# Performance work log

Measured on AMD Instinct MI355X. Metric: run time of the kernel, lower is better.

The kernel has to match this reference:

```python
import jax, jax.numpy as jnp
import numpy as np

NUM_HEADS = 16
DIM_HEAD = 64
DIM = 1024
SCALE = DIM ** (-0.5)  # NOTE: source scales by model dim, not dim_head


def setup_inputs() -> dict:
    key = jax.random.key(0)
    ks = jax.random.split(key, 6)
    b, n, d = 2, 2048, DIM
    return {
        "x": jax.random.normal(ks[0], (b, n, d), dtype=jnp.float32),
        "mask": jnp.ones((b, n), dtype=bool),
        "Wq": jax.random.normal(ks[1], (NUM_HEADS * DIM_HEAD, d), dtype=jnp.float32) * 0.02,
        "Wk": jax.random.normal(ks[2], (DIM_HEAD, d), dtype=jnp.float32) * 0.02,
        "Wv": jax.random.normal(ks[3], (DIM_HEAD, d), dtype=jnp.float32) * 0.02,
        "Wfc": jax.random.normal(ks[4], (d, NUM_HEADS * DIM_HEAD), dtype=jnp.float32) * 0.02,
        "bfc": jnp.zeros((d,), dtype=jnp.float32),
    }


def reference(x, mask, Wq, Wk, Wv, Wfc, bfc):
    b, n, _ = x.shape
    # projections (nn.Linear: y = x @ W.T)
    q = (x @ Wq.T).reshape(b, n, NUM_HEADS, DIM_HEAD).transpose(0, 2, 1, 3)  # b h n d
    k = x @ Wk.T  # b n d  (single shared MQA head)
    v = x @ Wv.T  # b n d
    energy = jnp.einsum("bhid,bjd->bhij", q, k) * SCALE  # b h i j
    mask_value = -jnp.finfo(energy.dtype).max
    # input mask: k_mask is all ones in source, so only query rows are masked
    q_mask = mask[:, None, :, None]  # b 1 i 1
    energy = jnp.where(q_mask, energy, mask_value)
    # causal mask: positions j > i are masked (i == j since self-attention)
    i = jnp.arange(n)
    causal = i[:, None] < i[None, :]  # True where future
    energy = jnp.where(causal[None, None, :, :], mask_value, energy)
    attn = jax.nn.softmax(energy, axis=-1)
    # dropout_rate = 0.0 -> identity
    out = jnp.einsum("bhij,bjd->bhid", attn, v)
    out = out.transpose(0, 2, 1, 3).reshape(b, n, NUM_HEADS * DIM_HEAD)
    return out @ Wfc.T + bfc
```

## Files before the change

### kernel.cpp

```cpp
#include <hip/hip_runtime.h>
#include <math.h>

#define NH 16
#define DH 64
#define DM 1024
#define NS 2048
#define BB 2
#define MR (BB * NS)
#define LDQ 1152
#define C_EXP 0.0450842201f

typedef unsigned short u16;
typedef __attribute__((ext_vector_type(8))) short short8;
typedef __attribute__((ext_vector_type(4))) float floatx4;
typedef __attribute__((ext_vector_type(4))) u16 u16x4;

#if __has_builtin(__builtin_amdgcn_exp2f)
#define EXP2(x) __builtin_amdgcn_exp2f(x)
#else
#define EXP2(x) exp2f(x)
#endif

#define MFMA16(a, b, c) __builtin_amdgcn_mfma_f32_16x16x32_bf16((a), (b), (c), 0, 0, 0)

static __device__ __forceinline__ u16 f2bf(float f) {
  union { float f; unsigned u; } v; v.f = f;
  unsigned r = v.u + 0x7fffu + ((v.u >> 16) & 1u);
  return (u16)(r >> 16);
}
static __device__ __forceinline__ u16 f2bf_fast(float f) {
  union { float f; unsigned u; } v; v.f = f;
  return (u16)((v.u + 0x8000u) >> 16);
}

#define GLDS16(gp, lp)                                                        \
  __builtin_amdgcn_global_load_lds(                                           \
      (const __attribute__((address_space(1))) void*)(const void*)(gp),       \
      (__attribute__((address_space(3))) void*)(void*)(lp), 16, 0, 0)

__global__ __launch_bounds__(256) void cast_all(
    const float* __restrict__ x, const float* __restrict__ wq,
    const float* __restrict__ wk, const float* __restrict__ wv,
    const float* __restrict__ wfc, u16* __restrict__ xb,
    u16* __restrict__ wqkvb, u16* __restrict__ wfcb) {
  const int NX = MR * DM / 4, NQ = DM * DM / 4, NK = DH * DM / 4;
  int id = blockIdx.x * 256 + threadIdx.x;
  const float* src;
  u16* dst;
  int off;
  if (id < NX) { src = x; dst = xb; off = id; }
  else if (id < NX + NQ) { src = wq; dst = wqkvb; off = id - NX; }
  else if (id < NX + NQ + NK) { src = wk; dst = wqkvb + (size_t)DM * DM; off = id - NX - NQ; }
  else if (id < NX + NQ + 2 * NK) { src = wv; dst = wqkvb + (size_t)(DM + DH) * DM; off = id - NX - NQ - NK; }
  else { src = wfc; dst = wfcb; off = id - NX - NQ - 2 * NK; }
  float4 f = ((const float4*)src)[off];
  u16x4 o;
  o[0] = f2bf(f.x); o[1] = f2bf(f.y); o[2] = f2bf(f.z); o[3] = f2bf(f.w);
  ((u16x4*)dst)[off] = o;
}

__global__ __launch_bounds__(256) void gemm64(
    const u16* __restrict__ A, const u16* __restrict__ W,
    const float* __restrict__ bias, void* __restrict__ Cout,
    u16* __restrict__ vT, int M, int N, int K, int ldc, int out_bf16,
    int v_by) {
  __shared__ u16 As[2][64 * 32];
  __shared__ u16 Ws[2][64 * 32];
  const int tid = threadIdx.x;
  const int lane = tid & 63;
  const int lr = lane & 15, quad = lane >> 4;
  const int wave = tid >> 6, wr = wave >> 1, wc = wave & 1;
  const int m0 = blockIdx.x * 64, n0 = blockIdx.y * 64;

  const int srow = tid >> 2;
  const int scg = (tid & 3) ^ ((srow >> 1) & 3);
  const u16* gA = A + (size_t)(m0 + srow) * K + scg * 8;
  const u16* gW = W + (size_t)(n0 + srow) * K + scg * 8;
  const int lo = wave * 512;

  floatx4 acc[2][2] = {};
  const int nt = K >> 5;

  GLDS16(gA, &As[0][lo]);
  GLDS16(gW, &Ws[0][lo]);

  for (int t = 0; t < nt; ++t) {
    __syncthreads();
    if (t + 1 < nt) {
      const int ko = (t + 1) << 5;
      const int nb = (t + 1) & 1;
      GLDS16(gA + ko, &As[nb][lo]);
      GLDS16(gW + ko, &Ws[nb][lo]);
    }
    const u16* as = As[t & 1];
    const u16* ws = Ws[t & 1];
    short8 af[2], wf[2];
#pragma unroll
    for (int mi = 0; mi < 2; ++mi) {
      int rr = wr * 32 + mi * 16 + lr;
      af[mi] = *(const short8*)&as[rr * 32 + ((quad ^ ((rr >> 1) & 3)) << 3)];
    }
#pragma unroll
    for (int nj = 0; nj < 2; ++nj) {
      int rc = wc * 32 + nj * 16 + lr;
      wf[nj] = *(const short8*)&ws[rc * 32 + ((quad ^ ((rc >> 1) & 3)) << 3)];
    }
#pragma unroll
    for (int mi = 0; mi < 2; ++mi)
#pragma unroll
      for (int nj = 0; nj < 2; ++nj)
        acc[mi][nj] = MFMA16(af[mi], wf[nj], acc[mi][nj]);
  }

  if (v_by >= 0 && (int)blockIdx.y == v_by) {
#pragma unroll
    for (int mi = 0; mi < 2; ++mi)
#pragma unroll
      for (int nj = 0; nj < 2; ++nj)
#pragma unroll
        for (int r = 0; r < 4; ++r)
          vT[(size_t)(wc * 32 + nj * 16 + lr) * MR + m0 + wr * 32 + mi * 16 +
             quad * 4 + r] = f2bf(acc[mi][nj][r]);
    return;
  }

#pragma unroll
  for (int mi = 0; mi < 2; ++mi) {
#pragma unroll
    for (int nj = 0; nj < 2; ++nj) {
      int col = n0 + wc * 32 + nj * 16 + lr;
      float badd = bias ? bias[col] : 0.f;
#pragma unroll
      for (int r = 0; r < 4; ++r) {
        int row = m0 + wr * 32 + mi * 16 + quad * 4 + r;
        float v = acc[mi][nj][r] + badd;
        if (out_bf16)
          ((u16*)Cout)[(size_t)row * ldc + col] = f2bf(v);
        else
          ((float*)Cout)[(size_t)row * ldc + col] = v;
      }
    }
  }
}

__global__ __launch_bounds__(128) void attn_mfma(
    const u16* __restrict__ qkv,
    const u16* __restrict__ vT,
    u16* __restrict__ aob) {
  __shared__ u16 Ks[2][64 * 64];
  __shared__ u16 Vt[2][64 * 64];
  __shared__ u16 Ps[2][16 * 72];

  const int b = blockIdx.z;
  const int p = blockIdx.x;
  const int head = blockIdx.y;
  const int tid = threadIdx.x;
  const int lane = tid & 63;
  const int lr = lane & 15, quad = lane >> 4;
  const int w = tid >> 6;
  const size_t rowb = (size_t)b * NS;
  const u16* kvK = qkv + rowb * LDQ + 1024;
  const u16* vTb = vT + rowb;

  int srow[4], scg[4];
#pragma unroll
  for (int g = 0; g < 4; ++g) {
    int ci = w * 256 + g * 64 + lane;
    srow[g] = ci >> 3;
    scg[g] = (ci & 7) ^ (srow[g] & 7);
  }

  for (int phase = 0; phase < 2; ++phase) {
    const int s = (phase == 0) ? (63 - p) : p;
    const int i0q = s * 32;
    const int ntp = (s >> 1) + 1;
    const int irow = i0q + w * 16 + quad * 4;

    const u16* qp = qkv + (rowb + i0q + w * 16 + lr) * LDQ + head * DH;
    short8 aq0 = *(const short8*)(qp + quad * 8);
    short8 aq1 = *(const short8*)(qp + 32 + quad * 8);

    floatx4 o[4] = {};
    float lacc[4] = {0.f, 0.f, 0.f, 0.f};

#pragma unroll
    for (int g = 0; g < 4; ++g)
      GLDS16(kvK + (size_t)srow[g] * LDQ + scg[g] * 8,
             &Ks[0][(w * 256 + g * 64) * 8]);
#pragma unroll
    for (int g = 0; g < 4; ++g)
      GLDS16(vTb + (size_t)srow[g] * MR + scg[g] * 8,
             &Vt[0][(w * 256 + g * 64) * 8]);

    for (int t = 0; t < ntp; ++t) {
      const int buf = t & 1;
      __syncthreads();

      if (t + 1 < ntp) {
        const int j0n = (t + 1) * 64;
        const int nb2 = buf ^ 1;
#pragma unroll
        for (int g = 0; g < 4; ++g)
          GLDS16(kvK + (size_t)(j0n + srow[g]) * LDQ + scg[g] * 8,
                 &Ks[nb2][(w * 256 + g * 64) * 8]);
#pragma unroll
        for (int g = 0; g < 4; ++g)
          GLDS16(vTb + (size_t)srow[g] * MR + j0n + scg[g] * 8,
                 &Vt[nb2][(w * 256 + g * 64) * 8]);
      }

      const int j0 = t * 64;
      const u16* ksb = Ks[buf];
      const u16* vtb = Vt[buf];
      floatx4 sv[4];
#pragma unroll
      for (int jb = 0; jb < 4; ++jb) {
        const int krow = jb * 16 + lr;
        short8 bk0 = *(const short8*)&ksb[krow * 64 + ((quad ^ (krow & 7)) << 3)];
        short8 bk1 = *(const short8*)&ksb[krow * 64 + (((4 + quad) ^ (krow & 7)) << 3)];
        floatx4 z = {};
        z = MFMA16(aq0, bk0, z);
        z = MFMA16(aq1, bk1, z);
        sv[jb] = z;
      }

      u16* Pw = Ps[w];
      const bool lastt = (t == ntp - 1);
#pragma unroll
      for (int jb = 0; jb < 4; ++jb) {
#pragma unroll
        for (int r = 0; r < 4; ++r) {
          float pe = EXP2(sv[jb][r] * C_EXP);
          if (lastt && (j0 + jb * 16 + lr > irow + r)) pe = 0.f;
          lacc[r] += pe;
          const int row = quad * 4 + r, colj = jb * 16 + lr;
          Pw[row * 72 + ((((colj >> 3) + (row >> 1)) & 7) << 3) + (colj & 7)] =
              f2bf_fast(pe);
        }
      }
      asm volatile("s_waitcnt lgkmcnt(0)" ::: "memory");
      short8 ap0 = *(const short8*)&Pw[lr * 72 + (((quad + (lr >> 1)) & 7) << 3)];
      short8 ap1 = *(const short8*)&Pw[lr * 72 + (((4 + quad + (lr >> 1)) & 7) << 3)];

#pragma unroll
      for (int nb = 0; nb < 4; ++nb) {
        const int d0 = nb * 16 + lr;
        short8 bv0 = *(const short8*)&vtb[d0 * 64 + ((quad ^ (d0 & 7)) << 3)];
        short8 bv1 = *(const short8*)&vtb[d0 * 64 + (((4 + quad) ^ (d0 & 7)) << 3)];
        o[nb] = MFMA16(ap0, bv0, o[nb]);
        o[nb] = MFMA16(ap1, bv1, o[nb]);
      }
    }

#pragma unroll
    for (int r = 0; r < 4; ++r) {
      float l = lacc[r];
      l += __shfl_xor(l, 1);
      l += __shfl_xor(l, 2);
      l += __shfl_xor(l, 4);
      l += __shfl_xor(l, 8);
      lacc[r] = l;
    }
#pragma unroll
    for (int nb = 0; nb < 4; ++nb)
#pragma unroll
      for (int r = 0; r < 4; ++r)
        aob[(rowb + irow + r) * DM + head * DH + nb * 16 + lr] =
            f2bf(o[nb][r] / lacc[r]);

    __syncthreads();
  }
}

extern "C" void kernel_launch(void* const* d_in, const int* in_sizes, int n_in,
                              void* d_out, int out_size, void* d_ws, size_t ws_size,
                              hipStream_t stream) {
  const float* x = (const float*)d_in[0];
  const float* Wq = (const float*)d_in[2];
  const float* Wk = (const float*)d_in[3];
  const float* Wv = (const float*)d_in[4];
  const float* Wfc = (const float*)d_in[5];
  const float* bfc = (const float*)d_in[6];

  u16* xb = (u16*)d_ws;
  u16* wqkvb = xb + (size_t)MR * DM;
  u16* wfcb = wqkvb + (size_t)LDQ * DM;
  u16* qkv = wfcb + (size_t)DM * DM;
  u16* vT = qkv + (size_t)MR * LDQ;
  u16* aob = xb;

  cast_all<<<dim3((MR * DM + DM * DM * 2 + DH * DM * 2) / 1024), dim3(256), 0,
             stream>>>(x, Wq, Wk, Wv, Wfc, xb, wqkvb, wfcb);
  gemm64<<<dim3(MR / 64, LDQ / 64), dim3(256), 0, stream>>>(
      xb, wqkvb, nullptr, qkv, vT, MR, LDQ, DM, LDQ, 1, 17);
  attn_mfma<<<dim3(32, NH, BB), dim3(128), 0, stream>>>(qkv, vT, aob);
  gemm64<<<dim3(MR / 64, DM / 64), dim3(256), 0, stream>>>(
      aob, wfcb, bfc, d_out, nullptr, MR, DM, DM, DM, 0, -1);
}
```

Baseline: 169.7 us.

## Enlarge GEMM tiles to 128x128 with triple-buffered async LDS pipeline

Replaces the 64x64 GEMM tile with a 128x128 tile where each wave computes a 64x64 subtile (4x4 MFMAs), raising arithmetic intensity per LDS load. Adds a three-stage shared-memory ring with explicit vmcnt waits so global loads for step t+2 overlap compute for step t. The V-transpose special case is remapped to the new column block (only the wc==1 waves store V). The grid shrinks to 32x9 and 32x8 blocks, which may underfill the GPU's compute units. Register and LDS use also grow.

```diff
diff --git a/kernel.cpp b/kernel.cpp
--- a/kernel.cpp
+++ b/kernel.cpp
@@ -59,80 +59,97 @@
   ((u16x4*)dst)[off] = o;
 }
 
-__global__ __launch_bounds__(256) void gemm64(
+__global__ __launch_bounds__(256) void gemm128(
     const u16* __restrict__ A, const u16* __restrict__ W,
     const float* __restrict__ bias, void* __restrict__ Cout,
-    u16* __restrict__ vT, int M, int N, int K, int ldc, int out_bf16,
-    int v_by) {
-  __shared__ u16 As[2][64 * 32];
-  __shared__ u16 Ws[2][64 * 32];
+    u16* __restrict__ vT, int K, int ldc, int out_bf16, int v_by) {
+  __shared__ u16 As[3][128 * 32];
+  __shared__ u16 Ws[3][128 * 32];
   const int tid = threadIdx.x;
   const int lane = tid & 63;
   const int lr = lane & 15, quad = lane >> 4;
   const int wave = tid >> 6, wr = wave >> 1, wc = wave & 1;
-  const int m0 = blockIdx.x * 64, n0 = blockIdx.y * 64;
-
-  const int srow = tid >> 2;
-  const int scg = (tid & 3) ^ ((srow >> 1) & 3);
-  const u16* gA = A + (size_t)(m0 + srow) * K + scg * 8;
-  const u16* gW = W + (size_t)(n0 + srow) * K + scg * 8;
-  const int lo = wave * 512;
-
-  floatx4 acc[2][2] = {};
+  const int m0 = blockIdx.x * 128, n0 = blockIdx.y * 128;
+
+  const u16* gA[2];
+  const u16* gW[2];
+  int lbase[2];
+#pragma unroll
+  for (int g = 0; g < 2; ++g) {
+    int ci = g * 256 + tid;
+    int row = ci >> 2, slot = ci & 3;
+    int gch = slot ^ ((row >> 1) & 3);
+    gA[g] = A + (size_t)(m0 + row) * K + gch * 8;
+    gW[g] = W + (size_t)(n0 + row) * K + gch * 8;
+    lbase[g] = (g * 256 + wave * 64) * 8;
+  }
+
+#define STAGE(t, b)                          \
+  do {                                       \
+    const int _ko = (t) << 5;                \
+    GLDS16(gA[0] + _ko, &As[b][lbase[0]]);   \
+    GLDS16(gA[1] + _ko, &As[b][lbase[1]]);   \
+    GLDS16(gW[0] + _ko, &Ws[b][lbase[0]]);   \
+    GLDS16(gW[1] + _ko, &Ws[b][lbase[1]]);   \
+  } while (0)
+
+  floatx4 acc[4][4] = {};
   const int nt = K >> 5;
 
-  GLDS16(gA, &As[0][lo]);
-  GLDS16(gW, &Ws[0][lo]);
+  STAGE(0, 0);
+  STAGE(1, 1);
 
   for (int t = 0; t < nt; ++t) {
-    __syncthreads();
-    if (t + 1 < nt) {
-      const int ko = (t + 1) << 5;
-      const int nb = (t + 1) & 1;
-      GLDS16(gA + ko, &As[nb][lo]);
-      GLDS16(gW + ko, &Ws[nb][lo]);
-    }
-    const u16* as = As[t & 1];
-    const u16* ws = Ws[t & 1];
-    short8 af[2], wf[2];
-#pragma unroll
-    for (int mi = 0; mi < 2; ++mi) {
-      int rr = wr * 32 + mi * 16 + lr;
+    if (t + 1 < nt)
+      asm volatile("s_waitcnt vmcnt(4)" ::: "memory");
+    else
+      asm volatile("s_waitcnt vmcnt(0)" ::: "memory");
+    __builtin_amdgcn_s_barrier();
+    asm volatile("" ::: "memory");
+    if (t + 2 < nt) STAGE(t + 2, (t + 2) % 3);
+
+    const u16* as = As[t % 3];
+    const u16* ws = Ws[t % 3];
+    short8 af[4], wf[4];
+#pragma unroll
+    for (int mi = 0; mi < 4; ++mi) {
+      int rr = wr * 64 + mi * 16 + lr;
       af[mi] = *(const short8*)&as[rr * 32 + ((quad ^ ((rr >> 1) & 3)) << 3)];
     }
 #pragma unroll
-    for (int nj = 0; nj < 2; ++nj) {
-      int rc = wc * 32 + nj * 16 + lr;
+    for (int nj = 0; nj < 4; ++nj) {
+      int rc = wc * 64 + nj * 16 + lr;
       wf[nj] = *(const short8*)&ws[rc * 32 + ((quad ^ ((rc >> 1) & 3)) << 3)];
     }
 #pragma unroll
-    for (int mi = 0; mi < 2; ++mi)
-#pragma unroll
-      for (int nj = 0; nj < 2; ++nj)
+    for (int mi = 0; mi < 4; ++mi)
+#pragma unroll
+      for (int nj = 0; nj < 4; ++nj)
         acc[mi][nj] = MFMA16(af[mi], wf[nj], acc[mi][nj]);
   }
-
-  if (v_by >= 0 && (int)blockIdx.y == v_by) {
-#pragma unroll
-    for (int mi = 0; mi < 2; ++mi)
-#pragma unroll
-      for (int nj = 0; nj < 2; ++nj)
+#undef STAGE
+
+  if (v_by == (int)blockIdx.y && wc == 1) {
+#pragma unroll
+    for (int mi = 0; mi < 4; ++mi)
+#pragma unroll
+      for (int nj = 0; nj < 4; ++nj)
 #pragma unroll
         for (int r = 0; r < 4; ++r)
-          vT[(size_t)(wc * 32 + nj * 16 + lr) * MR + m0 + wr * 32 + mi * 16 +
-             quad * 4 + r] = f2bf(acc[mi][nj][r]);
+          vT[(size_t)(nj * 16 + lr) * MR + m0 + wr * 64 + mi * 16 + quad * 4 +
+             r] = f2bf(acc[mi][nj][r]);
     return;
   }
 
 #pragma unroll
-  for (int mi = 0; mi < 2; ++mi) {
-#pragma unroll
-    for (int nj = 0; nj < 2; ++nj) {
-      int col = n0 + wc * 32 + nj * 16 + lr;
+  for (int mi = 0; mi < 4; ++mi) {
+#pragma unroll
+    for (int nj = 0; nj < 4; ++nj) {
+      int col = n0 + wc * 64 + nj * 16 + lr;
       float badd = bias ? bias[col] : 0.f;
 #pragma unroll
       for (int r = 0; r < 4; ++r) {
-        int row = m0 + wr * 32 + mi * 16 + quad * 4 + r;
+        int row = m0 + wr * 64 + mi * 16 + quad * 4 + r;
         float v = acc[mi][nj][r] + badd;
         if (out_bf16)
           ((u16*)Cout)[(size_t)row * ldc + col] = f2bf(v);
@@ -291,9 +308,9 @@
 
   cast_all<<<dim3((MR * DM + DM * DM * 2 + DH * DM * 2) / 1024), dim3(256), 0,
              stream>>>(x, Wq, Wk, Wv, Wfc, xb, wqkvb, wfcb);
-  gemm64<<<dim3(MR / 64, LDQ / 64), dim3(256), 0, stream>>>(
-      xb, wqkvb, nullptr, qkv, vT, MR, LDQ, DM, LDQ, 1, 17);
+  gemm128<<<dim3(MR / 128, LDQ / 128), dim3(256), 0, stream>>>(
+      xb, wqkvb, nullptr, qkv, vT, DM, LDQ, 1, 8);
   attn_mfma<<<dim3(32, NH, BB), dim3(128), 0, stream>>>(qkv, vT, aob);
-  gemm64<<<dim3(MR / 64, DM / 64), dim3(256), 0, stream>>>(
-      aob, wfcb, bfc, d_out, nullptr, MR, DM, DM, DM, 0, -1);
-}
+  gemm128<<<dim3(MR / 128, DM / 128), dim3(256), 0, stream>>>(
+      aob, wfcb, bfc, d_out, nullptr, DM, DM, 0, -1);
+}
```

Result: slower. 184.9 us (+9.0%).

## Share K/V tiles across four heads per attention block

Applied to the files above, without the earlier changes.

The attention kernel now handles four heads per block with 512 threads (8 waves) instead of one head per block with 128 threads. Because K and V are a single shared MQA head, each staged K/V tile in LDS now serves four heads, which cuts global K/V traffic and per-block load work by four. In exchange the grid shrinks to a quarter as many blocks, so fewer blocks are available to hide latency. All 8 waves also hit the same __syncthreads barrier each tile, which adds synchronisation cost.

```diff
diff --git a/kernel.cpp b/kernel.cpp
--- a/kernel.cpp
+++ b/kernel.cpp
@@ -143,54 +143,46 @@
   }
 }
 
-__global__ __launch_bounds__(128) void attn_mfma(
+__global__ __launch_bounds__(512) void attn_mfma(
     const u16* __restrict__ qkv,
     const u16* __restrict__ vT,
     u16* __restrict__ aob) {
   __shared__ u16 Ks[2][64 * 64];
   __shared__ u16 Vt[2][64 * 64];
-  __shared__ u16 Ps[2][16 * 72];
+  __shared__ u16 Ps[8][16 * 72];
 
   const int b = blockIdx.z;
   const int p = blockIdx.x;
-  const int head = blockIdx.y;
   const int tid = threadIdx.x;
   const int lane = tid & 63;
   const int lr = lane & 15, quad = lane >> 4;
   const int w = tid >> 6;
+  const int head = blockIdx.y * 4 + (w >> 1);
+  const int qh = (w & 1) * 16;
   const size_t rowb = (size_t)b * NS;
   const u16* kvK = qkv + rowb * LDQ + 1024;
   const u16* vTb = vT + rowb;
 
-  int srow[4], scg[4];
-#pragma unroll
-  for (int g = 0; g < 4; ++g) {
-    int ci = w * 256 + g * 64 + lane;
-    srow[g] = ci >> 3;
-    scg[g] = (ci & 7) ^ (srow[g] & 7);
-  }
+  const int ci = w * 64 + lane;
+  const int srow = ci >> 3;
+  const int scg = (ci & 7) ^ (srow & 7);
+  const int lo = w * 512;
 
   for (int phase = 0; phase < 2; ++phase) {
     const int s = (phase == 0) ? (63 - p) : p;
     const int i0q = s * 32;
     const int ntp = (s >> 1) + 1;
-    const int irow = i0q + w * 16 + quad * 4;
-
-    const u16* qp = qkv + (rowb + i0q + w * 16 + lr) * LDQ + head * DH;
+    const int irow = i0q + qh + quad * 4;
+
+    const u16* qp = qkv + (rowb + i0q + qh + lr) * LDQ + head * DH;
     short8 aq0 = *(const short8*)(qp + quad * 8);
     short8 aq1 = *(const short8*)(qp + 32 + quad * 8);
 
     floatx4 o[4] = {};
     float lacc[4] = {0.f, 0.f, 0.f, 0.f};
 
-#pragma unroll
-    for (int g = 0; g < 4; ++g)
-      GLDS16(kvK + (size_t)srow[g] * LDQ + scg[g] * 8,
-             &Ks[0][(w * 256 + g * 64) * 8]);
-#pragma unroll
-    for (int g = 0; g < 4; ++g)
-      GLDS16(vTb + (size_t)srow[g] * MR + scg[g] * 8,
-             &Vt[0][(w * 256 + g * 64) * 8]);
+    GLDS16(kvK + (size_t)srow * LDQ + scg * 8, &Ks[0][lo]);
+    GLDS16(vTb + (size_t)srow * MR + scg * 8, &Vt[0][lo]);
 
     for (int t = 0; t < ntp; ++t) {
       const int buf = t & 1;
@@ -199,14 +191,8 @@
       if (t + 1 < ntp) {
         const int j0n = (t + 1) * 64;
         const int nb2 = buf ^ 1;
-#pragma unroll
-        for (int g = 0; g < 4; ++g)
-          GLDS16(kvK + (size_t)(j0n + srow[g]) * LDQ + scg[g] * 8,
-                 &Ks[nb2][(w * 256 + g * 64) * 8]);
-#pragma unroll
-        for (int g = 0; g < 4; ++g)
-          GLDS16(vTb + (size_t)srow[g] * MR + j0n + scg[g] * 8,
-                 &Vt[nb2][(w * 256 + g * 64) * 8]);
+        GLDS16(kvK + (size_t)(j0n + srow) * LDQ + scg * 8, &Ks[nb2][lo]);
+        GLDS16(vTb + (size_t)srow * MR + j0n + scg * 8, &Vt[nb2][lo]);
       }
 
       const int j0 = t * 64;
@@ -293,7 +279,7 @@
              stream>>>(x, Wq, Wk, Wv, Wfc, xb, wqkvb, wfcb);
   gemm64<<<dim3(MR / 64, LDQ / 64), dim3(256), 0, stream>>>(
       xb, wqkvb, nullptr, qkv, vT, MR, LDQ, DM, LDQ, 1, 17);
-  attn_mfma<<<dim3(32, NH, BB), dim3(128), 0, stream>>>(qkv, vT, aob);
+  attn_mfma<<<dim3(32, NH / 4, BB), dim3(512), 0, stream>>>(qkv, vT, aob);
   gemm64<<<dim3(MR / 64, DM / 64), dim3(256), 0, stream>>>(
       aob, wfcb, bfc, d_out, nullptr, MR, DM, DM, DM, 0, -1);
 }
```

After: 164.5 us. 1.03x faster.
